# Kernel tuning notes

Hardware: AMD Instinct MI355X
Metric: run time of the kernel (lower is better)

## Reference

```python
import jax, jax.numpy as jnp
import numpy as np

B, N, C, H = 4, 1024, 768, 12
D = C // H
SCALE = D ** -0.5


def setup_inputs() -> dict:
    key = jax.random.key(0)
    k1, k2, k3, k4 = jax.random.split(key, 4)
    x1 = jax.random.normal(k1, (B, N, C), dtype=jnp.float32)
    x2 = jax.random.normal(k2, (B, N, C), dtype=jnp.float32)
    # shared (dual-stream) Linear2 weights, torch nn.Linear layout: [out, in]
    W_qkv = jax.random.normal(k3, (3 * C, C), dtype=jnp.float32) * (C ** -0.5)
    b_qkv = jnp.zeros((3 * C,), dtype=jnp.float32)
    W_proj = jax.random.normal(k4, (C, C), dtype=jnp.float32) * (C ** -0.5)
    b_proj = jnp.zeros((C,), dtype=jnp.float32)
    return {"x1": x1, "x2": x2, "W_qkv": W_qkv, "b_qkv": b_qkv,
            "W_proj": W_proj, "b_proj": b_proj}


def _split_qkv(x, W_qkv, b_qkv):
    qkv = (x @ W_qkv.T + b_qkv).reshape(B, N, 3, H, D)
    qkv = jnp.transpose(qkv, (2, 0, 3, 1, 4))  # [3,B,H,N,D]
    return qkv[0], qkv[1], qkv[2]


def reference(x1, x2, W_qkv, b_qkv, W_proj, b_proj):
    q1, k1, v1 = _split_qkv(x1, W_qkv, b_qkv)
    q2, k2, v2 = _split_qkv(x2, W_qkv, b_qkv)
    # two score maps, combined before a single shared softmax
    s1 = jnp.einsum("bhqd,bhkd->bhqk", q1 * SCALE, k1)
    s2 = jnp.einsum("bhqd,bhkd->bhqk", q2 * SCALE, k2)
    attn = jax.nn.softmax(s1 + s2, axis=-1)  # [B,H,N,N]
    # same attention matrix applied to both value streams
    o1 = jnp.einsum("bhqk,bhkd->bhqd", attn, v1)
    o2 = jnpum = jnp.einsum("bhqk,bhkd->bhqd", attn, v2) if False else jnp.einsum("bhqk,bhkd->bhqd", attn, v2)
    o1 = jnp.transpose(o1, (0, 2, 1, 3)).reshape(B, N, C)
    o2 = jnp.transpose(o2, (0, 2, 1, 3)).reshape(B, N, C)
    y1 = o1 @ W_proj.T + b_proj
    y2 = o2 @ W_proj.T + b_proj
    return y1, y2
```

## Files before the change

### kernel.cpp

```cpp
#include <hip/hip_runtime.h>
#include <hip/hip_bf16.h>


typedef __bf16 bf16x8 __attribute__((ext_vector_type(8)));
typedef __bf16 bf16x4 __attribute__((ext_vector_type(4)));
typedef float  f32x4  __attribute__((ext_vector_type(4)));

__device__ __forceinline__ bf16x8 cvt8(const float* p) {
    f32x4 f0 = *(const f32x4*)p;
    f32x4 f1 = *(const f32x4*)(p + 4);
    bf16x8 r;
    r[0] = (__bf16)f0[0]; r[1] = (__bf16)f0[1]; r[2] = (__bf16)f0[2]; r[3] = (__bf16)f0[3];
    r[4] = (__bf16)f1[0]; r[5] = (__bf16)f1[1]; r[6] = (__bf16)f1[2]; r[7] = (__bf16)f1[3];
    return r;
}

__device__ __forceinline__ void async16(const __bf16* g, __bf16* l) {
    __builtin_amdgcn_global_load_lds(
        (const __attribute__((address_space(1))) void*)g,
        (__attribute__((address_space(3))) void*)l, 16, 0, 0);
}

__global__ __launch_bounds__(256)
void cvt4_k(const float* __restrict__ x1, const float* __restrict__ x2,
            const float* __restrict__ wq, const float* __restrict__ wp,
            __bf16* __restrict__ xc, __bf16* __restrict__ wqc,
            __bf16* __restrict__ wpc)
{
    int bid = blockIdx.x;
    const float* src; __bf16* dst; int i;
    if (bid < 1536)      { src = x1; dst = xc;             i = (bid * 256 + threadIdx.x) * 8; }
    else if (bid < 3072) { src = x2; dst = xc + 3145728;   i = ((bid - 1536) * 256 + threadIdx.x) * 8; }
    else if (bid < 3936) { src = wq; dst = wqc;            i = ((bid - 3072) * 256 + threadIdx.x) * 8; }
    else                 { src = wp; dst = wpc;            i = ((bid - 3936) * 256 + threadIdx.x) * 8; }
    *(bf16x8*)(dst + i) = cvt8(src + i);
}

__global__ __launch_bounds__(256)
void cvt_k(const float* __restrict__ src, __bf16* __restrict__ dst, int n) {
    int i = (blockIdx.x * 256 + threadIdx.x) * 8;
    if (i < n) *(bf16x8*)(dst + i) = cvt8(src + i);
}

__global__ __launch_bounds__(256)
void gemm_qkv_s(const __bf16* __restrict__ Xc, const __bf16* __restrict__ Wq,
                const float* __restrict__ bias,
                __bf16* __restrict__ qo, __bf16* __restrict__ ko,
                __bf16* __restrict__ vo)
{
    constexpr int K = 768;
    __shared__ __bf16 As[4][128 * 32];
    __shared__ __bf16 Bs[4][128 * 32];

    const int t = threadIdx.x, w = t >> 6, lane = t & 63;
    const int l15 = lane & 15, quad = lane >> 4;
    const int wm = w >> 1, wn = w & 1;

    const int bid  = blockIdx.x;
    const int xcd  = bid & 7;
    const int i6   = bid >> 3;
    const int pair = i6 / 18;
    const int gx   = i6 - pair * 18;
    const int p    = xcd * 8 + pair;
    const int gy   = p & 31;
    const int st   = p >> 5;

    const int lrow = lane >> 2, lcol = (lane & 3) * 8;

    const __bf16* Ab = Xc + (size_t)st * 3145728 + (size_t)(gy * 128) * K;
    const __bf16* Bb = Wq + (size_t)(gx * 128) * K;

    f32x4 acc[4][4];
#pragma unroll
    for (int mi = 0; mi < 4; mi++)
#pragma unroll
        for (int ni = 0; ni < 4; ni++) acc[mi][ni] = f32x4{0.f, 0.f, 0.f, 0.f};

#define QSTAGE(BUF, KT)                                                         \
    do {                                                                        \
        const int _k0 = (KT) * 32;                                              \
        _Pragma("unroll")                                                       \
        for (int i = 0; i < 2; i++) {                                           \
            int r = w * 32 + i * 16 + lrow;                                     \
            async16(Ab + (size_t)r * K + _k0 + lcol, &As[BUF][r * 32 + lcol]);  \
            async16(Bb + (size_t)r * K + _k0 + lcol, &Bs[BUF][r * 32 + lcol]);  \
        }                                                                       \
    } while (0)

    QSTAGE(0, 0);
    QSTAGE(1, 1);

#pragma unroll 4
    for (int kt = 0; kt < 24; kt++) {
        const int cb = kt & 3;
        if (kt < 22) {
            QSTAGE((kt + 2) & 3, kt + 2);
            asm volatile("s_waitcnt vmcnt(8)" ::: "memory");
        } else if (kt == 22) {
            asm volatile("s_waitcnt vmcnt(4)" ::: "memory");
        } else {
            asm volatile("s_waitcnt vmcnt(0)" ::: "memory");
        }
        __builtin_amdgcn_s_barrier();
        __builtin_amdgcn_sched_barrier(0);

        bf16x8 af[4], bfr[4];
#pragma unroll
        for (int mi = 0; mi < 4; mi++)
            af[mi] = *(const bf16x8*)&As[cb][(wm * 64 + mi * 16 + l15) * 32 + quad * 8];
#pragma unroll
        for (int ni = 0; ni < 4; ni++)
            bfr[ni] = *(const bf16x8*)&Bs[cb][(wn * 64 + ni * 16 + l15) * 32 + quad * 8];
#pragma unroll
        for (int mi = 0; mi < 4; mi++)
#pragma unroll
            for (int ni = 0; ni < 4; ni++)
                acc[mi][ni] = __builtin_amdgcn_mfma_f32_16x16x32_bf16(af[mi], bfr[ni], acc[mi][ni], 0, 0, 0);
    }
#undef QSTAGE

    const int which = (gx * 128) / 768;

    if (which == 2) {
#pragma unroll
        for (int ni = 0; ni < 4; ni++) {
            int j = gx * 128 + wn * 64 + ni * 16 + l15;
            int c = j - 1536;
            int h = c >> 6, d = c & 63;
            float bj = bias[j];
#pragma unroll
            for (int mi = 0; mi < 4; mi++) {
                int row0 = gy * 128 + wm * 64 + mi * 16 + quad * 4;
                int b = row0 >> 10, tok0 = row0 & 1023;
                bf16x4 pv;
#pragma unroll
                for (int r = 0; r < 4; r++) pv[r] = (__bf16)(acc[mi][ni][r] + bj);
                *(bf16x4*)&vo[((size_t)((st * 4 + b) * 12 + h) * 64 + d) * 1024 + tok0] = pv;
            }
        }
    } else {
#pragma unroll
        for (int ni = 0; ni < 4; ni++) {
            int j     = gx * 128 + wn * 64 + ni * 16 + l15;
            int c     = j - which * 768;
            int h = c >> 6, d = c & 63;
            float bj  = bias[j];
#pragma unroll
            for (int mi = 0; mi < 4; mi++) {
#pragma unroll
                for (int r = 0; r < 4; r++) {
                    int row = gy * 128 + wm * 64 + mi * 16 + quad * 4 + r;
                    int b = row >> 10, tok = row & 1023;
                    float val = acc[mi][ni][r] + bj;
                    if (which == 0)
                        qo[((size_t)((st * 4 + b) * 12 + h) * 1024 + tok) * 64 + d] = (__bf16)(val * 0.125f);
                    else
                        ko[((size_t)((st * 4 + b) * 12 + h) * 1024 + tok) * 64 + d] = (__bf16)val;
                }
            }
        }
    }
}

__global__ __launch_bounds__(256)
void gemm_proj(const __bf16* __restrict__ A, const __bf16* __restrict__ Wp,
               const float* __restrict__ bias, float* __restrict__ out)
{
    constexpr int K = 768;
    __shared__ __bf16 As[4][128 * 32];
    __shared__ __bf16 Bs[4][128 * 32];

    const int t = threadIdx.x, w = t >> 6, lane = t & 63;
    const int l15 = lane & 15, quad = lane >> 4;
    const int wm = w >> 1, wn = w & 1;
    const int gx = blockIdx.x, gy = blockIdx.y;
    const int lrow = lane >> 2, lcol = (lane & 3) * 8;

    const __bf16* Ab = A  + (size_t)(gy * 128) * K;
    const __bf16* Bb = Wp + (size_t)(gx * 128) * K;

    f32x4 acc[4][4];
#pragma unroll
    for (int mi = 0; mi < 4; mi++)
#pragma unroll
        for (int ni = 0; ni < 4; ni++) acc[mi][ni] = f32x4{0.f, 0.f, 0.f, 0.f};

#define PSTAGE(BUF, KT)                                                         \
    do {                                                                        \
        const int _k0 = (KT) * 32;                                              \
        _Pragma("unroll")                                                       \
        for (int i = 0; i < 2; i++) {                                           \
            int r = w * 32 + i * 16 + lrow;                                     \
            async16(Ab + (size_t)r * K + _k0 + lcol, &As[BUF][r * 32 + lcol]);  \
            async16(Bb + (size_t)r * K + _k0 + lcol, &Bs[BUF][r * 32 + lcol]);  \
        }                                                                       \
    } while (0)

    PSTAGE(0, 0);
    PSTAGE(1, 1);

#pragma unroll 4
    for (int kt = 0; kt < 24; kt++) {
        const int cb = kt & 3;
        if (kt < 22) {
            PSTAGE((kt + 2) & 3, kt + 2);
            asm volatile("s_waitcnt vmcnt(8)" ::: "memory");
        } else if (kt == 22) {
            asm volatile("s_waitcnt vmcnt(4)" ::: "memory");
        } else {
            asm volatile("s_waitcnt vmcnt(0)" ::: "memory");
        }
        __builtin_amdgcn_s_barrier();
        __builtin_amdgcn_sched_barrier(0);

        bf16x8 af[4], bfr[4];
#pragma unroll
        for (int mi = 0; mi < 4; mi++)
            af[mi] = *(const bf16x8*)&As[cb][(wm * 64 + mi * 16 + l15) * 32 + quad * 8];
#pragma unroll
        for (int ni = 0; ni < 4; ni++)
            bfr[ni] = *(const bf16x8*)&Bs[cb][(wn * 64 + ni * 16 + l15) * 32 + quad * 8];
#pragma unroll
        for (int mi = 0; mi < 4; mi++)
#pragma unroll
            for (int ni = 0; ni < 4; ni++)
                acc[mi][ni] = __builtin_amdgcn_mfma_f32_16x16x32_bf16(af[mi], bfr[ni], acc[mi][ni], 0, 0, 0);
    }
#undef PSTAGE

#pragma unroll
    for (int ni = 0; ni < 4; ni++) {
        int col  = gx * 128 + wn * 64 + ni * 16 + l15;
        float bj = bias[col];
#pragma unroll
        for (int mi = 0; mi < 4; mi++)
#pragma unroll
            for (int r = 0; r < 4; r++) {
                int row = gy * 128 + wm * 64 + mi * 16 + quad * 4 + r;
                out[(size_t)row * 768 + col] = acc[mi][ni][r] + bj;
            }
    }
}

__global__ __launch_bounds__(128, 2)
void attn_k(const __bf16* __restrict__ qws, const __bf16* __restrict__ kws,
            const __bf16* __restrict__ vws, __bf16* __restrict__ ows)
{
    __shared__ __bf16 Ks[2][2][2][2][512];
    __shared__ __bf16 Vs[2][2][4][512];
    __shared__ __bf16 Ps[2][2][16 * 72];

    const int g  = blockIdx.x;
    const int qt = g / 48;
    const int bh = g % 48;
    const int b = bh / 12, h = bh % 12;
    const int t = threadIdx.x, w = t >> 6, lane = t & 63;
    const int l15 = lane & 15, quad = lane >> 4;

    const size_t head_off = (size_t)bh * 65536;
    const size_t ss       = (size_t)48 * 65536;

    bf16x8 qf[2][2][2];
#pragma unroll
    for (int set = 0; set < 2; set++)
#pragma unroll
        for (int s = 0; s < 2; s++)
#pragma unroll
            for (int kk = 0; kk < 2; kk++)
                qf[set][s][kk] = *(const bf16x8*)(qws + s * ss + head_off
                    + (size_t)(qt * 64 + w * 32 + set * 16 + l15) * 64 + kk * 32 + quad * 8);

    float lsum[2] = {0.f, 0.f};
    f32x4 accO[2][2][4];
#pragma unroll
    for (int set = 0; set < 2; set++)
#pragma unroll
        for (int s = 0; s < 2; s++)
#pragma unroll
            for (int mi = 0; mi < 4; mi++) accO[set][s][mi] = f32x4{0.f, 0.f, 0.f, 0.f};

    const __bf16* kbase = kws + head_off;
    const __bf16* vbase = vws + head_off;

#define STAGE_TILE(BUF, KEYB)                                                   \
    do {                                                                        \
        if (w == 0) {                                                           \
            _Pragma("unroll")                                                   \
            for (int i = 0; i < 8; i++) {                                       \
                const int s = i >> 2, kk = (i >> 1) & 1, mi = i & 1;            \
                async16(kbase + s * ss + (size_t)((KEYB) + mi * 16 + l15) * 64  \
                            + kk * 32 + quad * 8,                               \
                        &Ks[BUF][s][kk][mi][lane * 8]);                         \
            }                                                                   \
        } else {                                                                \
            _Pragma("unroll")                                                   \
            for (int i = 0; i < 8; i++) {                                       \
                const int s = i >> 2, mi = i & 3;                               \
                async16(vbase + s * ss + (size_t)(mi * 16 + l15) * 1024         \
                            + (KEYB) + quad * 8,                                \
                        &Vs[BUF][s][mi][lane * 8]);                             \
            }                                                                   \
        }                                                                       \
    } while (0)

    STAGE_TILE(0, 0);
    __syncthreads();

#pragma unroll 2
    for (int kt = 0; kt < 32; kt++) {
        const int cb = kt & 1, nb = cb ^ 1;

        if (kt < 31) STAGE_TILE(nb, (kt + 1) * 32);

        f32x4 accS[2][2];
#pragma unroll
        for (int set = 0; set < 2; set++)
#pragma unroll
            for (int mi = 0; mi < 2; mi++) accS[set][mi] = f32x4{0.f, 0.f, 0.f, 0.f};
        __builtin_amdgcn_s_setprio(1);
#pragma unroll
        for (int s = 0; s < 2; s++)
#pragma unroll
            for (int kk = 0; kk < 2; kk++) {
                bf16x8 kf0 = *(const bf16x8*)&Ks[cb][s][kk][0][lane * 8];
                bf16x8 kf1 = *(const bf16x8*)&Ks[cb][s][kk][1][lane * 8];
#pragma unroll
                for (int set = 0; set < 2; set++) {
                    accS[set][0] = __builtin_amdgcn_mfma_f32_16x16x32_bf16(kf0, qf[set][s][kk], accS[set][0], 0, 0, 0);
                    accS[set][1] = __builtin_amdgcn_mfma_f32_16x16x32_bf16(kf1, qf[set][s][kk], accS[set][1], 0, 0, 0);
                }
            }
        __builtin_amdgcn_s_setprio(0);

#pragma unroll
        for (int set = 0; set < 2; set++) {
            float rs = 0.f;
#pragma unroll
            for (int mi = 0; mi < 2; mi++) {
                bf16x4 pk;
#pragma unroll
                for (int r = 0; r < 4; r++) {
                    float pv = __expf(accS[set][mi][r]);
                    pk[r] = (__bf16)pv;
                    rs += pv;
                }
                *(bf16x4*)&Ps[w][set][l15 * 72 + mi * 16 + quad * 4] = pk;
            }
            lsum[set] += rs;
        }

        bf16x8 pa0 = *(const bf16x8*)&Ps[w][0][l15 * 72 + quad * 8];
        bf16x8 pa1 = *(const bf16x8*)&Ps[w][1][l15 * 72 + quad * 8];
        __builtin_amdgcn_s_setprio(1);
#pragma unroll
        for (int s = 0; s < 2; s++)
#pragma unroll
            for (int mi = 0; mi < 4; mi++) {
                bf16x8 vf = *(const bf16x8*)&Vs[cb][s][mi][lane * 8];
                accO[0][s][mi] = __builtin_amdgcn_mfma_f32_16x16x32_bf16(vf, pa0, accO[0][s][mi], 0, 0, 0);
                accO[1][s][mi] = __builtin_amdgcn_mfma_f32_16x16x32_bf16(vf, pa1, accO[1][s][mi], 0, 0, 0);
            }
        __builtin_amdgcn_s_setprio(0);

        __syncthreads();
    }
#undef STAGE_TILE

#pragma unroll
    for (int set = 0; set < 2; set++) {
        float l = lsum[set];
        l += __shfl_xor(l, 16);
        l += __shfl_xor(l, 32);
        float il = 1.f / l;

        const int tok = qt * 64 + w * 32 + set * 16 + l15;
#pragma unroll
        for (int s = 0; s < 2; s++)
#pragma unroll
            for (int mi = 0; mi < 4; mi++) {
                bf16x4 ov;
#pragma unroll
                for (int r = 0; r < 4; r++) ov[r] = (__bf16)(accO[set][s][mi][r] * il);
                *(bf16x4*)&ows[((size_t)((s * 4 + b) * 1024 + tok)) * 768
                               + h * 64 + mi * 16 + quad * 4] = ov;
            }
    }
}

extern "C" void kernel_launch(void* const* d_in, const int* in_sizes, int n_in,
                              void* d_out, int out_size, void* d_ws, size_t ws_size,
                              hipStream_t stream)
{
    const float* x1    = (const float*)d_in[0];
    const float* x2    = (const float*)d_in[1];
    const float* Wqkv  = (const float*)d_in[2];
    const float* bqkv  = (const float*)d_in[3];
    const float* Wproj = (const float*)d_in[4];
    const float* bproj = (const float*)d_in[5];
    float* out = (float*)d_out;

    const size_t qkv_elems = (size_t)2 * 4 * 12 * 1024 * 64;
    __bf16* q_ws = (__bf16*)d_ws;
    __bf16* k_ws = q_ws + qkv_elems;
    __bf16* v_ws = k_ws + qkv_elems;
    __bf16* pool = v_ws + qkv_elems;
    __bf16* Wqc  = pool + 3145728;
    __bf16* o_ws = pool;
    __bf16* Xc   = (__bf16*)d_out;

    const bool big = ws_size >= (size_t)(4 * qkv_elems + 589824) * sizeof(__bf16);
    __bf16* Wpc = big ? (pool + qkv_elems)
                      : q_ws;

    cvt4_k<<<big ? 4224 : 3936, 256, 0, stream>>>(x1, x2, Wqkv, Wproj, Xc, Wqc, Wpc);
    gemm_qkv_s<<<1152, 256, 0, stream>>>(Xc, Wqc, bqkv, q_ws, k_ws, v_ws);
    attn_k<<<768, 128, 0, stream>>>(q_ws, k_ws, v_ws, o_ws);
    if (!big) cvt_k<<<288, 256, 0, stream>>>(Wproj, Wpc, 589824);
    gemm_proj<<<dim3(6, 64), 256, 0, stream>>>(o_ws, Wpc, bproj, out);
}
```

Baseline: 211.9 us.

## Store GEMM tiles in MFMA-fragment order and shrink LDS ring to three stages

Both bf16 GEMM kernels now write each 16-row by 32-col subtile into LDS in lane order, so that every lane's MFMA fragment sits contiguously at lane*8 and the fragment reads become linear and conflict-free. The LDS ring drops from four buffers with prefetch distance two to three buffers with prefetch distance one, which cuts LDS use per block and may let more blocks share a CU. The cost is less load latency hidden per iteration and global loads whose per-lane addresses now span 16 rows per instruction.

```diff
diff --git a/kernel.cpp b/kernel.cpp
--- a/kernel.cpp
+++ b/kernel.cpp
@@ -49,8 +49,8 @@
                 __bf16* __restrict__ vo)
 {
     constexpr int K = 768;
-    __shared__ __bf16 As[4][128 * 32];
-    __shared__ __bf16 Bs[4][128 * 32];
+    __shared__ __bf16 As[3][128 * 32];
+    __shared__ __bf16 Bs[3][128 * 32];
 
     const int t = threadIdx.x, w = t >> 6, lane = t & 63;
     const int l15 = lane & 15, quad = lane >> 4;
@@ -65,7 +65,9 @@
     const int gy   = p & 31;
     const int st   = p >> 5;
 
-    const int lrow = lane >> 2, lcol = (lane & 3) * 8;
+    const int sgrp = w * 32;
+    const int srow = lane & 15;
+    const int scol = (lane >> 4) * 8;
 
     const __bf16* Ab = Xc + (size_t)st * 3145728 + (size_t)(gy * 128) * K;
     const __bf16* Bb = Wq + (size_t)(gx * 128) * K;
@@ -76,27 +78,26 @@
 #pragma unroll
         for (int ni = 0; ni < 4; ni++) acc[mi][ni] = f32x4{0.f, 0.f, 0.f, 0.f};
 
-#define QSTAGE(BUF, KT)                                                         \
-    do {                                                                        \
-        const int _k0 = (KT) * 32;                                              \
-        _Pragma("unroll")                                                       \
-        for (int i = 0; i < 2; i++) {                                           \
-            int r = w * 32 + i * 16 + lrow;                                     \
-            async16(Ab + (size_t)r * K + _k0 + lcol, &As[BUF][r * 32 + lcol]);  \
-            async16(Bb + (size_t)r * K + _k0 + lcol, &Bs[BUF][r * 32 + lcol]);  \
-        }                                                                       \
+#define QSTAGE(BUF, KT)                                                          \
+    do {                                                                         \
+        const int _k0 = (KT) * 32;                                               \
+        async16(Ab + (size_t)(sgrp + srow) * K + _k0 + scol,                     \
+                &As[BUF][sgrp * 32 + lane * 8]);                                 \
+        async16(Ab + (size_t)(sgrp + 16 + srow) * K + _k0 + scol,                \
+                &As[BUF][(sgrp + 16) * 32 + lane * 8]);                          \
+        async16(Bb + (size_t)(sgrp + srow) * K + _k0 + scol,                     \
+                &Bs[BUF][sgrp * 32 + lane * 8]);                                 \
+        async16(Bb + (size_t)(sgrp + 16 + srow) * K + _k0 + scol,                \
+                &Bs[BUF][(sgrp + 16) * 32 + lane * 8]);                          \
     } while (0)
 
     QSTAGE(0, 0);
-    QSTAGE(1, 1);
-
-#pragma unroll 4
+
+#pragma unroll 3
     for (int kt = 0; kt < 24; kt++) {
-        const int cb = kt & 3;
-        if (kt < 22) {
-            QSTAGE((kt + 2) & 3, kt + 2);
-            asm volatile("s_waitcnt vmcnt(8)" ::: "memory");
-        } else if (kt == 22) {
+        const int cb = kt % 3;
+        if (kt < 23) {
+            QSTAGE((kt + 1) % 3, kt + 1);
             asm volatile("s_waitcnt vmcnt(4)" ::: "memory");
         } else {
             asm volatile("s_waitcnt vmcnt(0)" ::: "memory");
@@ -107,10 +108,10 @@
         bf16x8 af[4], bfr[4];
 #pragma unroll
         for (int mi = 0; mi < 4; mi++)
-            af[mi] = *(const bf16x8*)&As[cb][(wm * 64 + mi * 16 + l15) * 32 + quad * 8];
+            af[mi] = *(const bf16x8*)&As[cb][(wm * 64 + mi * 16) * 32 + lane * 8];
 #pragma unroll
         for (int ni = 0; ni < 4; ni++)
-            bfr[ni] = *(const bf16x8*)&Bs[cb][(wn * 64 + ni * 16 + l15) * 32 + quad * 8];
+            bfr[ni] = *(const bf16x8*)&Bs[cb][(wn * 64 + ni * 16) * 32 + lane * 8];
 #pragma unroll
         for (int mi = 0; mi < 4; mi++)
 #pragma unroll
@@ -167,14 +168,17 @@
                const float* __restrict__ bias, float* __restrict__ out)
 {
     constexpr int K = 768;
-    __shared__ __bf16 As[4][128 * 32];
-    __shared__ __bf16 Bs[4][128 * 32];
+    __shared__ __bf16 As[3][128 * 32];
+    __shared__ __bf16 Bs[3][128 * 32];
 
     const int t = threadIdx.x, w = t >> 6, lane = t & 63;
     const int l15 = lane & 15, quad = lane >> 4;
     const int wm = w >> 1, wn = w & 1;
     const int gx = blockIdx.x, gy = blockIdx.y;
-    const int lrow = lane >> 2, lcol = (lane & 3) * 8;
+
+    const int sgrp = w * 32;
+    const int srow = lane & 15;
+    const int scol = (lane >> 4) * 8;
 
     const __bf16* Ab = A  + (size_t)(gy * 128) * K;
     const __bf16* Bb = Wp + (size_t)(gx * 128) * K;
@@ -185,27 +189,26 @@
 #pragma unroll
         for (int ni = 0; ni < 4; ni++) acc[mi][ni] = f32x4{0.f, 0.f, 0.f, 0.f};
 
-#define PSTAGE(BUF, KT)                                                         \
-    do {                                                                        \
-        const int _k0 = (KT) * 32;                                              \
-        _Pragma("unroll")                                                       \
-        for (int i = 0; i < 2; i++) {                                           \
-            int r = w * 32 + i * 16 + lrow;                                     \
-            async16(Ab + (size_t)r * K + _k0 + lcol, &As[BUF][r * 32 + lcol]);  \
-            async16(Bb + (size_t)r * K + _k0 + lcol, &Bs[BUF][r * 32 + lcol]);  \
-        }                                                                       \
+#define PSTAGE(BUF, KT)                                                          \
+    do {                                                                         \
+        const int _k0 = (KT) * 32;                                               \
+        async16(Ab + (size_t)(sgrp + srow) * K + _k0 + scol,                     \
+                &As[BUF][sgrp * 32 + lane * 8]);                                 \
+        async16(Ab + (size_t)(sgrp + 16 + srow) * K + _k0 + scol,                \
+                &As[BUF][(sgrp + 16) * 32 + lane * 8]);                          \
+        async16(Bb + (size_t)(sgrp + srow) * K + _k0 + scol,                     \
+                &Bs[BUF][sgrp * 32 + lane * 8]);                                 \
+        async16(Bb + (size_t)(sgrp + 16 + srow) * K + _k0 + scol,                \
+                &Bs[BUF][(sgrp + 16) * 32 + lane * 8]);                          \
     } while (0)
 
     PSTAGE(0, 0);
-    PSTAGE(1, 1);
-
-#pragma unroll 4
+
+#pragma unroll 3
     for (int kt = 0; kt < 24; kt++) {
-        const int cb = kt & 3;
-        if (kt < 22) {
-            PSTAGE((kt + 2) & 3, kt + 2);
-            asm volatile("s_waitcnt vmcnt(8)" ::: "memory");
-        } else if (kt == 22) {
+        const int cb = kt % 3;
+        if (kt < 23) {
+            PSTAGE((kt + 1) % 3, kt + 1);
             asm volatile("s_waitcnt vmcnt(4)" ::: "memory");
         } else {
             asm volatile("s_waitcnt vmcnt(0)" ::: "memory");
@@ -216,10 +219,10 @@
         bf16x8 af[4], bfr[4];
 #pragma unroll
         for (int mi = 0; mi < 4; mi++)
-            af[mi] = *(const bf16x8*)&As[cb][(wm * 64 + mi * 16 + l15) * 32 + quad * 8];
+            af[mi] = *(const bf16x8*)&As[cb][(wm * 64 + mi * 16) * 32 + lane * 8];
 #pragma unroll
         for (int ni = 0; ni < 4; ni++)
-            bfr[ni] = *(const bf16x8*)&Bs[cb][(wn * 64 + ni * 16 + l15) * 32 + quad * 8];
+            bfr[ni] = *(const bf16x8*)&Bs[cb][(wn * 64 + ni * 16) * 32 + lane * 8];
 #pragma unroll
         for (int mi = 0; mi < 4; mi++)
 #pragma unroll
```

Result: slower. 238.0 us (+12.3%).
